# Kernel tuning notes

Measured on AMD Instinct MI355X. Metric: run time of the kernel, lower is better.

Reference implementation:

```python
import jax, jax.numpy as jnp
import numpy as np

N_HEADS = 18
HEAD_DIM = 16
ROPE_THETA = 10000.0
SLIDING_WINDOW = 4096


def _rotate_half(x):
    half = x.shape[-1] // 2
    return jnp.concatenate([-x[..., half:], x[..., :half]], axis=-1)


def setup_inputs() -> dict:
    key = jax.random.key(0)
    k0, k1, k2, k3, k4 = jax.random.split(key, 5)
    B, S, H = 2, 2048, 288
    std = 0.02
    return {
        "hidden_states": jax.random.normal(k0, (B, S, H), dtype=jnp.float32),
        "Wq": jax.random.normal(k1, (H, H), dtype=jnp.float32) * std,
        "Wk": jax.random.normal(k2, (H, H), dtype=jnp.float32) * std,
        "Wv": jax.random.normal(k3, (H, H), dtype=jnp.float32) * std,
        "Wo": jax.random.normal(k4, (H, H), dtype=jnp.float32) * std,
    }


def reference(hidden_states, Wq, Wk, Wv, Wo):
    B, S, H = hidden_states.shape
    nH, D = N_HEADS, HEAD_DIM

    # QKV projections (nn.Linear: y = x @ W.T), reshape to [B, nH, S, D]
    def proj(W):
        return jnp.einsum("bsh,oh->bso", hidden_states, W).reshape(B, S, nH, D).transpose(0, 2, 1, 3)

    q, k, v = proj(Wq), proj(Wk), proj(Wv)

    # Rotary embedding: position_ids = arange(S)
    pos = jnp.arange(S, dtype=jnp.float32)
    inv_freq = 1.0 / (ROPE_THETA ** (jnp.arange(0, D, 2, dtype=jnp.float32) / D))
    freqs = pos[:, None] * inv_freq[None, :]            # [S, D/2]
    emb = jnp.concatenate([freqs, freqs], axis=-1)      # [S, D]
    cos = jnp.cos(emb)[None, None, :, :]                # [1, 1, S, D]
    sin = jnp.sin(emb)[None, None, :, :]
    q = q * cos + _rotate_half(q) * sin
    k = k * cos + _rotate_half(k) * sin

    # num_key_value_groups = 1 -> repeat_kv is identity.
    scores = jnp.einsum("bhqd,bhkd->bhqk", q, k) / jnp.sqrt(jnp.float32(D))

    # Sliding-window causal mask: attend iff 0 <= i - j < window
    i = jnp.arange(S)[:, None]
    j = jnp.arange(S)[None, :]
    allowed = (j <= i) & (i - j < SLIDING_WINDOW)       # [S, S]
    neg = jnp.finfo(scores.dtype).min
    scores = jnp.where(allowed[None, None, :, :], scores, neg)

    attn = jax.nn.softmax(scores.astype(jnp.float32), axis=-1).astype(q.dtype)
    out = jnp.einsum("bhqk,bhkd->bhqd", attn, v)        # [B, nH, S, D]
    out = out.transpose(0, 2, 1, 3).reshape(B, S, H)
    return jnp.einsum("bsh,oh->bso", out, Wo)
```

## Files before the change

kernel.cpp:

```cpp
#include <hip/hip_runtime.h>
#include <hip/hip_bf16.h>
#include <math.h>

#define H_DIM 288
#define NHEADS 18
#define HEAD_D 16
#define SEQ 2048
#define BATCH 2
#define M_TOT (BATCH*SEQ)
#define XCNT (M_TOT*H_DIM)
#define WCNT (H_DIM*H_DIM)
#define NUNITS 10368
#define NQUNITS 2304

typedef _Float16 f16_t;
typedef __attribute__((ext_vector_type(2))) _Float16 half2v;
typedef __attribute__((ext_vector_type(4))) _Float16 half4v;
typedef __attribute__((ext_vector_type(8))) _Float16 half8v;
typedef __attribute__((ext_vector_type(4))) float   float4v;

__global__ __launch_bounds__(256) void cvt_f16(
    const float* __restrict__ X,
    const float* __restrict__ Wq, const float* __restrict__ Wk,
    const float* __restrict__ Wv, const float* __restrict__ Wo,
    f16_t* __restrict__ Xf, f16_t* __restrict__ Wf)
{
    int idx = blockIdx.x * 256 + threadIdx.x;
    const int X4 = XCNT/4, W4 = WCNT/4;
    if (idx >= X4 + 4*W4) return;
    const float* src; f16_t* dst; int off;
    if (idx < X4) { src = X; dst = Xf; off = idx; }
    else {
        int r = idx - X4;
        int wz = r / W4; off = r - wz*W4;
        src = (wz==0) ? Wq : (wz==1) ? Wk : (wz==2) ? Wv : Wo;
        dst = Wf + (size_t)wz*WCNT;
    }
    float4 v = ((const float4*)src)[off];
    half4v h; h[0]=(f16_t)v.x; h[1]=(f16_t)v.y; h[2]=(f16_t)v.z; h[3]=(f16_t)v.w;
    ((half4v*)dst)[off] = h;
}

__global__ __launch_bounds__(64) void qkv_mfma(
    const f16_t* __restrict__ Xf, const f16_t* __restrict__ Wf,
    f16_t* __restrict__ Q16, f16_t* __restrict__ K16, f16_t* __restrict__ Vt)
{
    const int bx = blockIdx.x;
    const int z  = bx/6;
    const int n0 = (bx - z*6)*48;
    const int m0 = blockIdx.y*32;
    const int lane = threadIdx.x & 63;
    const int n = lane & 15, quad = lane >> 4;

    const f16_t* W = Wf + (size_t)z*WCNT;

    float4v acc[2][3];
    #pragma unroll
    for (int mt = 0; mt < 2; mt++)
        #pragma unroll
        for (int nt = 0; nt < 3; nt++)
            acc[mt][nt] = (float4v){0.f,0.f,0.f,0.f};

    for (int k0 = 0; k0 < H_DIM; k0 += 32) {
        half8v a[2], b[3];
        #pragma unroll
        for (int mt = 0; mt < 2; mt++)
            a[mt] = *(const half8v*)(Xf + (size_t)(m0 + mt*16 + n)*H_DIM + k0 + quad*8);
        #pragma unroll
        for (int nt = 0; nt < 3; nt++)
            b[nt] = *(const half8v*)(W + (size_t)(n0 + nt*16 + n)*H_DIM + k0 + quad*8);
        #pragma unroll
        for (int mt = 0; mt < 2; mt++)
            #pragma unroll
            for (int nt = 0; nt < 3; nt++)
                acc[mt][nt] = __builtin_amdgcn_mfma_f32_16x16x32_f16(a[mt], b[nt], acc[mt][nt], 0, 0, 0);
    }

    if (z < 2) {
        f16_t* dst = (z == 0) ? Q16 : K16;
        const float invf_rev = exp2f(-1.6609640474436813f * (float)(n & 7))
                             * 0.15915494309189535f;
        #pragma unroll
        for (int mt = 0; mt < 2; mt++) {
            #pragma unroll
            for (int r = 0; r < 4; r++) {
                int m = m0 + mt*16 + quad*4 + r;
                int bb = m >> 11, s = m & (SEQ - 1);
                float rev = (float)s * invf_rev;
                float fr = rev - floorf(rev);
                float sn = __builtin_amdgcn_sinf(fr);
                float c  = __builtin_amdgcn_cosf(fr);
                #pragma unroll
                for (int nt = 0; nt < 3; nt++) {
                    float own = acc[mt][nt][r];
                    float par = __shfl_xor(own, 8, 64);
                    float val = (n & 8) ? fmaf(own, c, par*sn) : fmaf(own, c, -par*sn);
                    if (z == 0) val *= 0.36067376022224085f;
                    int head = (n0 >> 4) + nt;
                    dst[((size_t)((bb*NHEADS + head)*SEQ) + s)*HEAD_D + n] = (f16_t)val;
                }
            }
        }
    } else {
        #pragma unroll
        for (int mt = 0; mt < 2; mt++)
            #pragma unroll
            for (int nt = 0; nt < 3; nt++)
                #pragma unroll
                for (int r = 0; r < 4; r++) {
                    int m = m0 + mt*16 + quad*4 + r;
                    int bb = m >> 11, s = m & (SEQ - 1);
                    int head = (n0 >> 4) + nt;
                    Vt[(size_t)(bb*NHEADS + head)*(SEQ*HEAD_D)
                       + (size_t)(s >> 4)*256 + n*16 + (s & 15)] = (f16_t)acc[mt][nt][r];
                }
    }
}

__device__ __forceinline__ half4v pack4(const float p[4]) {
    half2v ab = __builtin_bit_cast(half2v, __builtin_amdgcn_cvt_pkrtz(p[0], p[1]));
    half2v cd = __builtin_bit_cast(half2v, __builtin_amdgcn_cvt_pkrtz(p[2], p[3]));
    half4v o; o[0]=ab[0]; o[1]=ab[1]; o[2]=cd[0]; o[3]=cd[1];
    return o;
}

__global__ __launch_bounds__(256) void attn_part(
    const f16_t* __restrict__ Q16, const f16_t* __restrict__ K16,
    const f16_t* __restrict__ Vt,
    half4v* __restrict__ accbuf, f16_t* __restrict__ lbuf)
{
    const int unit = blockIdx.x*4 + (threadIdx.x >> 6);
    const int lane = threadIdx.x & 63;
    const int n = lane & 15, quad = lane >> 4;

    const int bh = unit / 288;
    const int rem = unit - bh*288;
    int g, t0;
    if      (rem < 8)   { g=0; t0=rem;     }
    else if (rem < 24)  { g=1; t0=rem-8;   }
    else if (rem < 48)  { g=2; t0=rem-24;  }
    else if (rem < 80)  { g=3; t0=rem-48;  }
    else if (rem < 120) { g=4; t0=rem-80;  }
    else if (rem < 168) { g=5; t0=rem-120; }
    else if (rem < 224) { g=6; t0=rem-168; }
    else                { g=7; t0=rem-224; }
    const int qd = t0 / (g+1);
    const int qp = 8*g + qd;
    const int chunk = t0 - qd*(g+1);
    const int q0 = qp*32;

    half4v qb0 = *(const half4v*)(Q16 + ((size_t)bh*SEQ + q0 + n)*HEAD_D + quad*4);
    half4v qb1 = *(const half4v*)(Q16 + ((size_t)bh*SEQ + q0 + 16 + n)*HEAD_D + quad*4);
    const f16_t* Kb = K16 + (size_t)bh * SEQ * HEAD_D;
    const f16_t* Vb = Vt  + (size_t)bh * SEQ * HEAD_D;
    const int loff = n*16 + quad*4;

    const float4v zero = {0.f, 0.f, 0.f, 0.f};
    float4v acc0 = zero, acc1 = zero;
    float l0 = 0.f, l1 = 0.f;

    const int lim0 = 2*qp, lim1 = 2*qp + 1;
    const int ktlo = chunk*16;
    const int kthi = min(ktlo + 15, lim1);

    if (ktlo + 15 < lim0) {
        half4v KA[16], VA[16];
        #pragma unroll
        for (int i = 0; i < 16; i++) {
            KA[i] = *(const half4v*)(Kb + (size_t)(ktlo + i)*256 + loff);
            VA[i] = *(const half4v*)(Vb + (size_t)(ktlo + i)*256 + loff);
        }
        #pragma unroll
        for (int i = 0; i < 16; i++) {
            float4v s1 = __builtin_amdgcn_mfma_f32_16x16x16f16(KA[i], qb1, zero, 0, 0, 0);
            float4v s0 = __builtin_amdgcn_mfma_f32_16x16x16f16(KA[i], qb0, zero, 0, 0, 0);
            float p1[4], p0[4];
            #pragma unroll
            for (int r = 0; r < 4; r++) { p1[r] = __builtin_amdgcn_exp2f(s1[r]); p0[r] = __builtin_amdgcn_exp2f(s0[r]); }
            l1 += (p1[0]+p1[1]) + (p1[2]+p1[3]);
            l0 += (p0[0]+p0[1]) + (p0[2]+p0[3]);
            acc1 = __builtin_amdgcn_mfma_f32_16x16x16f16(VA[i], pack4(p1), acc1, 0, 0, 0);
            acc0 = __builtin_amdgcn_mfma_f32_16x16x16f16(VA[i], pack4(p0), acc0, 0, 0, 0);
        }
    } else {
        int kt = ktlo;
        half4v ka = *(const half4v*)(Kb + (size_t)kt*256 + loff);
        half4v va = *(const half4v*)(Vb + (size_t)kt*256 + loff);
        for (; kt <= kthi; kt++) {
            half4v kan, van;
            if (kt < kthi) {
                kan = *(const half4v*)(Kb + (size_t)(kt+1)*256 + loff);
                van = *(const half4v*)(Vb + (size_t)(kt+1)*256 + loff);
            }
            {
                float4v s = __builtin_amdgcn_mfma_f32_16x16x16f16(ka, qb1, zero, 0, 0, 0);
                float p[4];
                #pragma unroll
                for (int r = 0; r < 4; r++) {
                    float e = __builtin_amdgcn_exp2f(s[r]);
                    p[r] = (kt == lim1 && quad*4 + r > n) ? 0.0f : e;
                }
                l1 += (p[0]+p[1]) + (p[2]+p[3]);
                acc1 = __builtin_amdgcn_mfma_f32_16x16x16f16(va, pack4(p), acc1, 0, 0, 0);
            }
            if (kt <= lim0) {
                float4v s = __builtin_amdgcn_mfma_f32_16x16x16f16(ka, qb0, zero, 0, 0, 0);
                float p[4];
                #pragma unroll
                for (int r = 0; r < 4; r++) {
                    float e = __builtin_amdgcn_exp2f(s[r]);
                    p[r] = (kt == lim0 && quad*4 + r > n) ? 0.0f : e;
                }
                l0 += (p[0]+p[1]) + (p[2]+p[3]);
                acc0 = __builtin_amdgcn_mfma_f32_16x16x16f16(va, pack4(p), acc0, 0, 0, 0);
            }
            ka = kan; va = van;
        }
    }

    float a0f[4] = {acc0[0], acc0[1], acc0[2], acc0[3]};
    float a1f[4] = {acc1[0], acc1[1], acc1[2], acc1[3]};
    accbuf[((size_t)unit*2 + 0)*64 + lane] = pack4(a0f);
    accbuf[((size_t)unit*2 + 1)*64 + lane] = pack4(a1f);
    lbuf[((size_t)unit*2 + 0)*64 + lane] = (f16_t)l0;
    lbuf[((size_t)unit*2 + 1)*64 + lane] = (f16_t)l1;
}

__global__ __launch_bounds__(256) void attn_red(
    const half4v* __restrict__ accbuf, const f16_t* __restrict__ lbuf,
    f16_t* __restrict__ Of)
{
    const int wid = blockIdx.x*4 + (threadIdx.x >> 6);
    const int lane = threadIdx.x & 63;
    const int n = lane & 15, quad = lane >> 4;
    const int bh = wid >> 6, qp = wid & 63;
    const int b = bh / NHEADS, h = bh - b*NHEADS;
    const int g = qp >> 3, j = qp & 7;
    const int nch = g + 1;
    const int ubase = bh*288 + qp + 4*g*(g-1) + g*j;

    #pragma unroll
    for (int t = 0; t < 2; t++) {
        float4 a = {0.f, 0.f, 0.f, 0.f};
        float l = 0.f;
        for (int c = 0; c < nch; c++) {
            size_t idx = ((size_t)(ubase + c)*2 + t)*64 + lane;
            half4v v = accbuf[idx];
            a.x += (float)v[0]; a.y += (float)v[1];
            a.z += (float)v[2]; a.w += (float)v[3];
            l += (float)lbuf[idx];
        }
        l += __shfl_xor(l, 16, 64);
        l += __shfl_xor(l, 32, 64);
        float inv = 1.0f / l;
        half4v o;
        o[0]=(f16_t)(a.x*inv); o[1]=(f16_t)(a.y*inv);
        o[2]=(f16_t)(a.z*inv); o[3]=(f16_t)(a.w*inv);
        *(half4v*)(Of + (size_t)(b*SEQ + qp*32 + t*16 + n)*H_DIM + h*HEAD_D + quad*4) = o;
    }
}

__global__ __launch_bounds__(64) void out_mfma(
    const f16_t* __restrict__ Of, const f16_t* __restrict__ Wo16,
    float* __restrict__ C)
{
    const int n0 = blockIdx.x * 48;
    const int m0 = blockIdx.y * 32;
    const int lane = threadIdx.x & 63;
    const int n = lane & 15, quad = lane >> 4;

    float4v acc[2][3];
    #pragma unroll
    for (int mt = 0; mt < 2; mt++)
        #pragma unroll
        for (int nt = 0; nt < 3; nt++)
            acc[mt][nt] = (float4v){0.f,0.f,0.f,0.f};

    for (int k0 = 0; k0 < H_DIM; k0 += 32) {
        half8v a[2], b[3];
        #pragma unroll
        for (int mt = 0; mt < 2; mt++)
            a[mt] = *(const half8v*)(Of + (size_t)(m0 + mt*16 + n)*H_DIM + k0 + quad*8);
        #pragma unroll
        for (int nt = 0; nt < 3; nt++)
            b[nt] = *(const half8v*)(Wo16 + (size_t)(n0 + nt*16 + n)*H_DIM + k0 + quad*8);
        #pragma unroll
        for (int mt = 0; mt < 2; mt++)
            #pragma unroll
            for (int nt = 0; nt < 3; nt++)
                acc[mt][nt] = __builtin_amdgcn_mfma_f32_16x16x32_f16(a[mt], b[nt], acc[mt][nt], 0, 0, 0);
    }
    #pragma unroll
    for (int mt = 0; mt < 2; mt++)
        #pragma unroll
        for (int nt = 0; nt < 3; nt++)
            #pragma unroll
            for (int r = 0; r < 4; r++) {
                int m = m0 + mt*16 + quad*4 + r;
                C[(size_t)m*H_DIM + n0 + nt*16 + n] = acc[mt][nt][r];
            }
}

extern "C" void kernel_launch(void* const* d_in, const int* in_sizes, int n_in,
                              void* d_out, int out_size, void* d_ws, size_t ws_size,
                              hipStream_t stream)
{
    const float* Xh = (const float*)d_in[0];
    const float* Wq = (const float*)d_in[1];
    const float* Wk = (const float*)d_in[2];
    const float* Wv = (const float*)d_in[3];
    const float* Wo = (const float*)d_in[4];
    float* out = (float*)d_out;

    f16_t* Xf  = (f16_t*)d_ws;
    f16_t* Wf  = Xf + XCNT;
    f16_t* Q16 = Wf + 4*(size_t)WCNT;
    f16_t* K16 = Q16 + XCNT;
    f16_t* Vt  = K16 + XCNT;
    f16_t* Of  = Vt + XCNT;
    half4v* accbuf = (half4v*)(Of + XCNT);
    f16_t*  lbuf   = (f16_t*)(accbuf + (size_t)NUNITS*2*64);

    const int total4 = (XCNT + 4*WCNT)/4;
    cvt_f16<<<dim3((total4 + 255)/256), 256, 0, stream>>>(Xh, Wq, Wk, Wv, Wo, Xf, Wf);
    qkv_mfma<<<dim3(18, 128), 64, 0, stream>>>(Xf, Wf, Q16, K16, Vt);
    attn_part<<<dim3(NUNITS/4), 256, 0, stream>>>(Q16, K16, Vt, accbuf, lbuf);
    attn_red<<<dim3(NQUNITS/4), 256, 0, stream>>>(accbuf, lbuf, Of);
    out_mfma<<<dim3(6, 128), 64, 0, stream>>>(Of, Wf + 3*(size_t)WCNT, out);
}
```

Measured before the change: 112.7 us.

## Fuse fp16 conversion into QKV GEMM and merge reduction with output projection

Drops the separate fp32-to-fp16 conversion kernel. The QKV and output GEMMs now load fp32 inputs and weights and convert them in registers. The attention partial reduction is fused with the output projection: each 384-thread block reduces 32 query rows across all heads into shared memory, then runs the Wo GEMM from LDS. This removes two launches and the Xf and Of round-trips through global memory. In exchange it reads twice as many fp32 bytes and repeats the weight conversion per block, and the fused kernel runs only 128 blocks, which may underfill the GPU.

```diff
diff --git a/kernel.cpp b/kernel.cpp
--- a/kernel.cpp
+++ b/kernel.cpp
@@ -11,7 +11,6 @@
 #define XCNT (M_TOT*H_DIM)
 #define WCNT (H_DIM*H_DIM)
 #define NUNITS 10368
-#define NQUNITS 2304
 
 typedef _Float16 f16_t;
 typedef __attribute__((ext_vector_type(2))) _Float16 half2v;
@@ -19,30 +18,26 @@
 typedef __attribute__((ext_vector_type(8))) _Float16 half8v;
 typedef __attribute__((ext_vector_type(4))) float   float4v;
 
-__global__ __launch_bounds__(256) void cvt_f16(
+__device__ __forceinline__ half8v cvt8(const float* __restrict__ p) {
+    float4 x0 = *(const float4*)p;
+    float4 x1 = *(const float4*)(p + 4);
+    half8v h;
+    h[0]=(f16_t)x0.x; h[1]=(f16_t)x0.y; h[2]=(f16_t)x0.z; h[3]=(f16_t)x0.w;
+    h[4]=(f16_t)x1.x; h[5]=(f16_t)x1.y; h[6]=(f16_t)x1.z; h[7]=(f16_t)x1.w;
+    return h;
+}
+
+__device__ __forceinline__ half4v pack4(const float p[4]) {
+    half2v ab = __builtin_bit_cast(half2v, __builtin_amdgcn_cvt_pkrtz(p[0], p[1]));
+    half2v cd = __builtin_bit_cast(half2v, __builtin_amdgcn_cvt_pkrtz(p[2], p[3]));
+    half4v o; o[0]=ab[0]; o[1]=ab[1]; o[2]=cd[0]; o[3]=cd[1];
+    return o;
+}
+
+__global__ __launch_bounds__(64) void qkv_mfma(
     const float* __restrict__ X,
     const float* __restrict__ Wq, const float* __restrict__ Wk,
-    const float* __restrict__ Wv, const float* __restrict__ Wo,
-    f16_t* __restrict__ Xf, f16_t* __restrict__ Wf)
-{
-    int idx = blockIdx.x * 256 + threadIdx.x;
-    const int X4 = XCNT/4, W4 = WCNT/4;
-    if (idx >= X4 + 4*W4) return;
-    const float* src; f16_t* dst; int off;
-    if (idx < X4) { src = X; dst = Xf; off = idx; }
-    else {
-        int r = idx - X4;
-        int wz = r / W4; off = r - wz*W4;
-        src = (wz==0) ? Wq : (wz==1) ? Wk : (wz==2) ? Wv : Wo;
-        dst = Wf + (size_t)wz*WCNT;
-    }
-    float4 v = ((const float4*)src)[off];
-    half4v h; h[0]=(f16_t)v.x; h[1]=(f16_t)v.y; h[2]=(f16_t)v.z; h[3]=(f16_t)v.w;
-    ((half4v*)dst)[off] = h;
-}
-
-__global__ __launch_bounds__(64) void qkv_mfma(
-    const f16_t* __restrict__ Xf, const f16_t* __restrict__ Wf,
+    const float* __restrict__ Wv,
     f16_t* __restrict__ Q16, f16_t* __restrict__ K16, f16_t* __restrict__ Vt)
 {
     const int bx = blockIdx.x;
@@ -52,7 +47,7 @@
     const int lane = threadIdx.x & 63;
     const int n = lane & 15, quad = lane >> 4;
 
-    const f16_t* W = Wf + (size_t)z*WCNT;
+    const float* W = (z==0) ? Wq : (z==1) ? Wk : Wv;
 
     float4v acc[2][3];
     #pragma unroll
@@ -65,10 +60,10 @@
         half8v a[2], b[3];
         #pragma unroll
         for (int mt = 0; mt < 2; mt++)
-            a[mt] = *(const half8v*)(Xf + (size_t)(m0 + mt*16 + n)*H_DIM + k0 + quad*8);
-        #pragma unroll
-        for (int nt = 0; nt < 3; nt++)
-            b[nt] = *(const half8v*)(W + (size_t)(n0 + nt*16 + n)*H_DIM + k0 + quad*8);
+            a[mt] = cvt8(X + (size_t)(m0 + mt*16 + n)*H_DIM + k0 + quad*8);
+        #pragma unroll
+        for (int nt = 0; nt < 3; nt++)
+            b[nt] = cvt8(W + (size_t)(n0 + nt*16 + n)*H_DIM + k0 + quad*8);
         #pragma unroll
         for (int mt = 0; mt < 2; mt++)
             #pragma unroll
@@ -117,13 +112,6 @@
     }
 }
 
-__device__ __forceinline__ half4v pack4(const float p[4]) {
-    half2v ab = __builtin_bit_cast(half2v, __builtin_amdgcn_cvt_pkrtz(p[0], p[1]));
-    half2v cd = __builtin_bit_cast(half2v, __builtin_amdgcn_cvt_pkrtz(p[2], p[3]));
-    half4v o; o[0]=ab[0]; o[1]=ab[1]; o[2]=cd[0]; o[3]=cd[1];
-    return o;
-}
-
 __global__ __launch_bounds__(256) void attn_part(
     const f16_t* __restrict__ Q16, const f16_t* __restrict__ K16,
     const f16_t* __restrict__ Vt,
@@ -226,49 +214,47 @@
     lbuf[((size_t)unit*2 + 1)*64 + lane] = (f16_t)l1;
 }
 
-__global__ __launch_bounds__(256) void attn_red(
+__global__ __launch_bounds__(384) void red_out(
     const half4v* __restrict__ accbuf, const f16_t* __restrict__ lbuf,
-    f16_t* __restrict__ Of)
+    const float* __restrict__ Wo, float* __restrict__ C)
 {
-    const int wid = blockIdx.x*4 + (threadIdx.x >> 6);
+    __shared__ f16_t Ot[32][296];
+    const int y = blockIdx.x;
+    const int b = y >> 6, qp = y & 63;
+    const int w = threadIdx.x >> 6;
     const int lane = threadIdx.x & 63;
     const int n = lane & 15, quad = lane >> 4;
-    const int bh = wid >> 6, qp = wid & 63;
-    const int b = bh / NHEADS, h = bh - b*NHEADS;
     const int g = qp >> 3, j = qp & 7;
     const int nch = g + 1;
-    const int ubase = bh*288 + qp + 4*g*(g-1) + g*j;
 
     #pragma unroll
-    for (int t = 0; t < 2; t++) {
-        float4 a = {0.f, 0.f, 0.f, 0.f};
-        float l = 0.f;
-        for (int c = 0; c < nch; c++) {
-            size_t idx = ((size_t)(ubase + c)*2 + t)*64 + lane;
-            half4v v = accbuf[idx];
-            a.x += (float)v[0]; a.y += (float)v[1];
-            a.z += (float)v[2]; a.w += (float)v[3];
-            l += (float)lbuf[idx];
-        }
-        l += __shfl_xor(l, 16, 64);
-        l += __shfl_xor(l, 32, 64);
-        float inv = 1.0f / l;
-        half4v o;
-        o[0]=(f16_t)(a.x*inv); o[1]=(f16_t)(a.y*inv);
-        o[2]=(f16_t)(a.z*inv); o[3]=(f16_t)(a.w*inv);
-        *(half4v*)(Of + (size_t)(b*SEQ + qp*32 + t*16 + n)*H_DIM + h*HEAD_D + quad*4) = o;
-    }
-}
-
-__global__ __launch_bounds__(64) void out_mfma(
-    const f16_t* __restrict__ Of, const f16_t* __restrict__ Wo16,
-    float* __restrict__ C)
-{
-    const int n0 = blockIdx.x * 48;
-    const int m0 = blockIdx.y * 32;
-    const int lane = threadIdx.x & 63;
-    const int n = lane & 15, quad = lane >> 4;
-
+    for (int hh = 0; hh < 3; hh++) {
+        const int h = w*3 + hh;
+        const int bh = b*NHEADS + h;
+        const int ubase = bh*288 + qp + 4*g*(g-1) + g*j;
+        #pragma unroll
+        for (int t = 0; t < 2; t++) {
+            float4 a = {0.f, 0.f, 0.f, 0.f};
+            float l = 0.f;
+            for (int c = 0; c < nch; c++) {
+                size_t idx = ((size_t)(ubase + c)*2 + t)*64 + lane;
+                half4v v = accbuf[idx];
+                a.x += (float)v[0]; a.y += (float)v[1];
+                a.z += (float)v[2]; a.w += (float)v[3];
+                l += (float)lbuf[idx];
+            }
+            l += __shfl_xor(l, 16, 64);
+            l += __shfl_xor(l, 32, 64);
+            float inv = 1.0f / l;
+            half4v o;
+            o[0]=(f16_t)(a.x*inv); o[1]=(f16_t)(a.y*inv);
+            o[2]=(f16_t)(a.z*inv); o[3]=(f16_t)(a.w*inv);
+            *(half4v*)&Ot[t*16 + n][h*16 + quad*4] = o;
+        }
+    }
+    __syncthreads();
+
+    const int n0 = w*48;
     float4v acc[2][3];
     #pragma unroll
     for (int mt = 0; mt < 2; mt++)
@@ -277,18 +263,18 @@
             acc[mt][nt] = (float4v){0.f,0.f,0.f,0.f};
 
     for (int k0 = 0; k0 < H_DIM; k0 += 32) {
-        half8v a[2], b[3];
-        #pragma unroll
-        for (int mt = 0; mt < 2; mt++)
-            a[mt] = *(const half8v*)(Of + (size_t)(m0 + mt*16 + n)*H_DIM + k0 + quad*8);
-        #pragma unroll
-        for (int nt = 0; nt < 3; nt++)
-            b[nt] = *(const half8v*)(Wo16 + (size_t)(n0 + nt*16 + n)*H_DIM + k0 + quad*8);
+        half8v a[2], bb[3];
+        #pragma unroll
+        for (int mt = 0; mt < 2; mt++)
+            a[mt] = *(const half8v*)&Ot[mt*16 + n][k0 + quad*8];
+        #pragma unroll
+        for (int nt = 0; nt < 3; nt++)
+            bb[nt] = cvt8(Wo + (size_t)(n0 + nt*16 + n)*H_DIM + k0 + quad*8);
         #pragma unroll
         for (int mt = 0; mt < 2; mt++)
             #pragma unroll
             for (int nt = 0; nt < 3; nt++)
-                acc[mt][nt] = __builtin_amdgcn_mfma_f32_16x16x32_f16(a[mt], b[nt], acc[mt][nt], 0, 0, 0);
+                acc[mt][nt] = __builtin_amdgcn_mfma_f32_16x16x32_f16(a[mt], bb[nt], acc[mt][nt], 0, 0, 0);
     }
     #pragma unroll
     for (int mt = 0; mt < 2; mt++)
@@ -296,7 +282,7 @@
         for (int nt = 0; nt < 3; nt++)
             #pragma unroll
             for (int r = 0; r < 4; r++) {
-                int m = m0 + mt*16 + quad*4 + r;
+                int m = y*32 + mt*16 + quad*4 + r;
                 C[(size_t)m*H_DIM + n0 + nt*16 + n] = acc[mt][nt][r];
             }
 }
@@ -312,19 +298,13 @@
     const float* Wo = (const float*)d_in[4];
     float* out = (float*)d_out;
 
-    f16_t* Xf  = (f16_t*)d_ws;
-    f16_t* Wf  = Xf + XCNT;
-    f16_t* Q16 = Wf + 4*(size_t)WCNT;
+    f16_t* Q16 = (f16_t*)d_ws;
     f16_t* K16 = Q16 + XCNT;
     f16_t* Vt  = K16 + XCNT;
-    f16_t* Of  = Vt + XCNT;
-    half4v* accbuf = (half4v*)(Of + XCNT);
+    half4v* accbuf = (half4v*)(Vt + XCNT);
     f16_t*  lbuf   = (f16_t*)(accbuf + (size_t)NUNITS*2*64);
 
-    const int total4 = (XCNT + 4*WCNT)/4;
-    cvt_f16<<<dim3((total4 + 255)/256), 256, 0, stream>>>(Xh, Wq, Wk, Wv, Wo, Xf, Wf);
-    qkv_mfma<<<dim3(18, 128), 64, 0, stream>>>(Xf, Wf, Q16, K16, Vt);
+    qkv_mfma<<<dim3(18, 128), 64, 0, stream>>>(Xh, Wq, Wk, Wv, Q16, K16, Vt);
     attn_part<<<dim3(NUNITS/4), 256, 0, stream>>>(Q16, K16, Vt, accbuf, lbuf);
-    attn_red<<<dim3(NQUNITS/4), 256, 0, stream>>>(accbuf, lbuf, Of);
-    out_mfma<<<dim3(6, 128), 64, 0, stream>>>(Of, Wf + 3*(size_t)WCNT, out);
-}
+    red_out<<<dim3(128), 384, 0, stream>>>(accbuf, lbuf, Wo, out);
+}
```

New measurement: 140.9 us. 25.0% more time.
